# Performance work log

Hardware: AMD Instinct MI355X
Metric: run time of the kernel (lower is better)

Reference implementation:

```python
import jax, jax.numpy as jnp
import numpy as np

B, N, F, H = 8, 384, 64, 128
LN_EPS = 1e-5


def setup_inputs() -> dict:
    key = jax.random.key(0)
    ks = jax.random.split(key, 8)
    s = 0.1
    return {
        "inputs": jax.random.normal(ks[0], (B, N, F), jnp.float32),
        "positions": jax.random.normal(ks[1], (B, N, 3), jnp.float32),
        "vW1": jax.random.normal(ks[2], (2, H), jnp.float32) * s,
        "vb1": jnp.zeros((H,), jnp.float32),
        "vg": jnp.ones((H,), jnp.float32),
        "vbeta": jnp.zeros((H,), jnp.float32),
        "vW2": jax.random.normal(ks[3], (H, F), jnp.float32) * s,
        "vb2": jnp.zeros((F,), jnp.float32),
        "sW1": jax.random.normal(ks[4], (F, H), jnp.float32) * s,
        "sb1": jnp.zeros((H,), jnp.float32),
        "sW2": jax.random.normal(ks[5], (H, 1), jnp.float32) * s,
        "sb2": jnp.zeros((1,), jnp.float32),
    }


def reference(inputs, positions, vW1, vb1, vg, vbeta, vW2, vb2, sW1, sb1, sW2, sb2):
    # --- pairwise geometric invariants (rank=2, 'single'): [dot, |cross|] ---
    # left[b,i,j] = pos[b,j], right[b,i,j] = pos[b,i]
    dot = jnp.einsum("bjd,bid->bij", positions, positions)            # (B,N,N)
    cross = jnp.cross(positions[:, None, :, :], positions[:, :, None, :])
    cnorm = jnp.sqrt(jnp.sum(cross * cross, axis=-1))                  # (B,N,N)
    invariants = jnp.stack([dot, cnorm], axis=-1)                      # (B,N,N,2)

    # --- value_net: Linear -> LayerNorm -> ReLU -> Linear ---
    h = invariants @ vW1 + vb1                                         # (B,N,N,H)
    mu = jnp.mean(h, axis=-1, keepdims=True)
    var = jnp.mean((h - mu) ** 2, axis=-1, keepdims=True)
    h = (h - mu) * jax.lax.rsqrt(var + LN_EPS) * vg + vbeta
    invariant_values = jax.nn.relu(h) @ vW2 + vb2                      # (B,N,N,F)

    # --- merge ('mean') and join ('mean') ---
    merged = (inputs[:, None, :, :] + inputs[:, :, None, :]) * 0.5     # (B,N,N,F)
    joined = (invariant_values + merged) * 0.5                         # (B,N,N,F)

    # --- score_net: Linear -> ReLU -> Linear ---
    scores = jax.nn.relu(joined @ sW1 + sb1) @ sW2 + sb2               # (B,N,N,1)

    # --- flattened softmax over all N*N pairs, weighted sum over dim=-2 ---
    att = jax.nn.softmax(scores.reshape(scores.shape[0], -1), axis=-1)
    att = att.reshape(scores.shape)                                    # (B,N,N,1)
    x = jnp.sum(att * joined, axis=-2)                                 # (B,N,F)
    return x, att
```

## Files before the change

### kernel.cpp

```cpp
#include <hip/hip_runtime.h>
#include <hip/hip_bf16.h>
#include <math.h>

#define B_ 8
#define N_ 384
#define F_ 64
#define H_ 128
#define LN_EPS 1e-5f

typedef _Float16 f16;
typedef f16 f16x2 __attribute__((ext_vector_type(2)));
typedef f16 f16x4 __attribute__((ext_vector_type(4)));
typedef f16 f16x8 __attribute__((ext_vector_type(8)));
typedef float f32x4v __attribute__((ext_vector_type(4)));

static __device__ __forceinline__ f16x2 u2h(unsigned int u) {
    union { unsigned int u; f16x2 h; } c; c.u = u; return c.h;
}
static __device__ __forceinline__ unsigned int h2u(f16 a, f16 b) {
    union { f16x2 h; unsigned int u; } c; c.h = (f16x2){a, b}; return c.u;
}
static __device__ __forceinline__ unsigned int x2u(f16x2 h) {
    union { f16x2 h; unsigned int u; } c; c.h = h; return c.u;
}
static __device__ __forceinline__ f16x2 pk2(float a, float b) {
    auto r = __builtin_amdgcn_cvt_pkrtz(a, b);
    union { decltype(r) r; f16x2 h; } c; c.r = r; return c.h;
}

static __device__ __forceinline__ void perm_idx(int m, int& u, int& n0) {
    int h4 = (m >> 1) & 3, mf = m >> 3, p = m & 1;
    u = h4 * 16 + mf * 2 + p;
    n0 = mf * 16 + h4 * 4 + 2 * p;
}

__global__ __launch_bounds__(128) void k_prep(
    const float* __restrict__ inp, const float* __restrict__ sW1,
    const float* __restrict__ vb2, const float* __restrict__ sb1,
    const float* __restrict__ vW2, const float* __restrict__ vW1,
    const float* __restrict__ vb1, const float* __restrict__ vg,
    const float* __restrict__ vbeta, const float* __restrict__ sW2,
    unsigned int* __restrict__ t16, unsigned short* __restrict__ W2hT,
    unsigned int* __restrict__ coeffP, float* __restrict__ scal,
    unsigned int* __restrict__ sw16) {
    __shared__ float red[128];
    __shared__ float caS[128], cbS[128], ccS[128];
    const int bx = blockIdx.x;
    const int tid = threadIdx.x;

    if (bx < B_ * N_) {
        int row = bx, n = tid;
        float acc = 0.f;
#pragma unroll
        for (int f = 0; f < F_; ++f)
            acc = fmaf(0.25f * (inp[row * F_ + f] + vb2[f]), sW1[f * H_ + n], acc);
        red[n] = acc + 0.5f * sb1[n];
        __syncthreads();
        if (tid < 64) {
            int u, n0; perm_idx(tid, u, n0);
            t16[row * 64 + u] = h2u((f16)red[n0], (f16)red[n0 + 1]);
        }
        return;
    }
    if (bx < B_ * N_ + 128) {
        int idx = (bx - B_ * N_) * 128 + tid;
        int k = idx >> 7, n = idx & 127;
        float acc = 0.f;
#pragma unroll
        for (int f = 0; f < F_; ++f) acc = fmaf(vW2[k * F_ + f], sW1[f * H_ + n], acc);
        f16 hv = (f16)(0.5f * acc);
        W2hT[n * H_ + k] = *reinterpret_cast<unsigned short*>(&hv);
        return;
    }

    const int d = tid;
    float a = vW1[d], bb = vW1[H_ + d], c = vb1[d];
    float mA, mB, mC, Saa, Sbb, Scc, Sab, Sac, Sbc;
    float ca, cb, cc;
#define BMEAN(OUT, VAL)                                                  \
    red[d] = (VAL); __syncthreads();                                     \
    for (int st = 64; st > 0; st >>= 1) {                                \
        if (d < st) red[d] += red[d + st];                               \
        __syncthreads();                                                 \
    }                                                                    \
    OUT = red[0] * (1.f / 128.f); __syncthreads();

    BMEAN(mA, a); BMEAN(mB, bb); BMEAN(mC, c);
    ca = a - mA; cb = bb - mB; cc = c - mC;
    caS[d] = ca * vg[d]; cbS[d] = cb * vg[d]; ccS[d] = cc * vg[d];
    BMEAN(Saa, ca * ca); BMEAN(Sbb, cb * cb); BMEAN(Scc, cc * cc);
    BMEAN(Sab, ca * cb); BMEAN(Sac, ca * cc); BMEAN(Sbc, cb * cc);
#undef BMEAN
    __syncthreads();
    if (d < 64) {
        int d0 = 2 * d;
        coeffP[d]       = h2u((f16)caS[d0], (f16)caS[d0 + 1]);
        coeffP[64 + d]  = h2u((f16)cbS[d0], (f16)cbS[d0 + 1]);
        coeffP[128 + d] = h2u((f16)ccS[d0], (f16)ccS[d0 + 1]);
        coeffP[192 + d] = h2u((f16)vbeta[d0], (f16)vbeta[d0 + 1]);
        int u, n0; perm_idx(d, u, n0);
        sw16[u] = h2u((f16)sW2[n0], (f16)sW2[n0 + 1]);
    }
    if (d == 0) {
        scal[0] = Saa; scal[1] = Sbb; scal[2] = Scc;
        scal[3] = Sab; scal[4] = Sac; scal[5] = Sbc;
    }
}

#define VW2_OFF 32768
__global__ __launch_bounds__(256) void k_scores(
    const float* __restrict__ pos, const unsigned int* __restrict__ coeffP,
    const float* __restrict__ scal, const unsigned short* __restrict__ W2hT,
    const float* __restrict__ vW2, const unsigned int* __restrict__ t16,
    const unsigned int* __restrict__ sw16, const float* __restrict__ sb2,
    float* __restrict__ scores, float* __restrict__ rowsum,
    float* __restrict__ xpart) {
    __shared__ __align__(16) char smem[65536];

    const int tid = threadIdx.x;
    const int b = blockIdx.y;
    const int w = tid >> 6, lane = tid & 63;
    const int i = blockIdx.x * 4 + w;
    const int ln = lane & 15, h4 = lane >> 4;

#pragma unroll
    for (int s = 0; s < 8; ++s) {
        int idx = tid + s * 256;
        int n = idx >> 4, c = idx & 15;
        uint4 v = *(const uint4*)(W2hT + n * H_ + c * 8);
        *(uint4*)(smem + ((n * 256 + c * 16) ^ ((n & 7) << 4))) = v;
    }
#pragma unroll
    for (int s = 0; s < 8; ++s) {
        int idx = tid + s * 256;
        uint4 v = *(const uint4*)((const float*)vW2 + idx * 4);
        *(uint4*)(smem + VW2_OFF + idx * 16) = v;
    }
    __syncthreads();

    uint4 cagR[4], cbgR[4], ccgR[4], vbR[4];
#pragma unroll
    for (int kc = 0; kc < 4; ++kc) {
        cagR[kc] = *(const uint4*)(coeffP + kc * 16 + h4 * 4);
        cbgR[kc] = *(const uint4*)(coeffP + 64 + kc * 16 + h4 * 4);
        ccgR[kc] = *(const uint4*)(coeffP + 128 + kc * 16 + h4 * 4);
        vbR[kc]  = *(const uint4*)(coeffP + 192 + kc * 16 + h4 * 4);
    }
    f32x4v acc0[8];
    {
        const unsigned int* tiP = t16 + (size_t)(b * N_ + i) * 64 + h4 * 16;
#pragma unroll
        for (int s = 0; s < 4; ++s) {
            uint4 v = *(const uint4*)(tiP + s * 4);
            f16x2 a0 = u2h(v.x), a1 = u2h(v.y), a2 = u2h(v.z), a3 = u2h(v.w);
            acc0[s * 2][0] = (float)a0[0]; acc0[s * 2][1] = (float)a0[1];
            acc0[s * 2][2] = (float)a1[0]; acc0[s * 2][3] = (float)a1[1];
            acc0[s * 2 + 1][0] = (float)a2[0]; acc0[s * 2 + 1][1] = (float)a2[1];
            acc0[s * 2 + 1][2] = (float)a3[0]; acc0[s * 2 + 1][3] = (float)a3[1];
        }
    }
    uint2 swR[8];
#pragma unroll
    for (int mf = 0; mf < 8; ++mf)
        swR[mf] = *(const uint2*)(sw16 + h4 * 16 + mf * 2);

    const float Saa = scal[0], Sbb = scal[1], Scc = scal[2];
    const float Sab = scal[3], Sac = scal[4], Sbc = scal[5];
    const float sb2v = sb2[0];

    const float* pi = pos + (size_t)(b * N_ + i) * 3;
    const float ax = pi[0], ay = pi[1], az = pi[2];
    float* scoreRow = scores + (size_t)(b * N_ + i) * N_;

    float s_run = 0.f;
    unsigned int accPh[16];
#pragma unroll
    for (int k = 0; k < 16; ++k) accPh[k] = 0u;

    auto makeBF = [&](float bx_, float by_, float bz_, f16x8 (&bF)[4]) {
        float dotv = ax * bx_ + ay * by_ + az * bz_;
        float cx = ay * bz_ - az * by_;
        float cy = az * bx_ - ax * bz_;
        float cz = ax * by_ - ay * bx_;
        float cns = cx * cx + cy * cy + cz * cz;
        float cn = sqrtf(cns);
        float var = Saa * dotv * dotv + Sbb * cns + Scc +
                    2.f * (Sab * dotv * cn + Sac * dotv + Sbc * cn);
        float rstd = rsqrtf(var + LN_EPS);
        f16 d2 = (f16)(dotv * rstd), c2 = (f16)(cn * rstd), r2 = (f16)rstd;
        f16x2 D2 = {d2, d2}, C2 = {c2, c2}, R2 = {r2, r2};
        const f16x2 Z = {(f16)0.f, (f16)0.f};
#pragma unroll
        for (int kc = 0; kc < 4; ++kc) {
            f16x2 vp0 = __builtin_elementwise_max(D2 * u2h(cagR[kc].x) + (C2 * u2h(cbgR[kc].x) + (R2 * u2h(ccgR[kc].x) + u2h(vbR[kc].x))), Z);
            f16x2 vp1 = __builtin_elementwise_max(D2 * u2h(cagR[kc].y) + (C2 * u2h(cbgR[kc].y) + (R2 * u2h(ccgR[kc].y) + u2h(vbR[kc].y))), Z);
            f16x2 vp2 = __builtin_elementwise_max(D2 * u2h(cagR[kc].z) + (C2 * u2h(cbgR[kc].z) + (R2 * u2h(ccgR[kc].z) + u2h(vbR[kc].z))), Z);
            f16x2 vp3 = __builtin_elementwise_max(D2 * u2h(cagR[kc].w) + (C2 * u2h(cbgR[kc].w) + (R2 * u2h(ccgR[kc].w) + u2h(vbR[kc].w))), Z);
            f16x4 q01 = __builtin_shufflevector(vp0, vp1, 0, 1, 2, 3);
            f16x4 q23 = __builtin_shufflevector(vp2, vp3, 0, 1, 2, 3);
            bF[kc] = __builtin_shufflevector(q01, q23, 0, 1, 2, 3, 4, 5, 6, 7);
        }
    };

    float bx, by, bz;
    auto body = [&](int jt, f16x8 (&bFu)[4], f16x8 (&bFb)[4]) {
        const int j0 = jt * 16;

        const unsigned int* tjP = t16 + (size_t)(b * N_ + j0 + ln) * 64 + h4 * 16;
        uint4 tj0 = *(const uint4*)(tjP);
        uint4 tj1 = *(const uint4*)(tjP + 4);
        uint4 tj2 = *(const uint4*)(tjP + 8);
        uint4 tj3 = *(const uint4*)(tjP + 12);

        f32x4v acc[8];
        {
            const int kb = (h4 * 16) ^ ((ln & 7) << 4);
#pragma unroll
            for (int mf = 0; mf < 8; ++mf) {
                f16x8 aFr = *(const f16x8*)(smem + (mf * 16 + ln) * 256 + kb);
                acc[mf] = __builtin_amdgcn_mfma_f32_16x16x32_f16(aFr, bFu[0], acc0[mf], 0, 0, 0);
            }
        }
#pragma unroll
        for (int kc = 1; kc < 4; ++kc) {
            const int kb = (kc * 64 + h4 * 16) ^ ((ln & 7) << 4);
#pragma unroll
            for (int mf = 0; mf < 8; ++mf) {
                f16x8 aFr = *(const f16x8*)(smem + (mf * 16 + ln) * 256 + kb);
                acc[mf] = __builtin_amdgcn_mfma_f32_16x16x32_f16(aFr, bFu[kc], acc[mf], 0, 0, 0);
            }
        }

        {
            float gx = bx, gy = by, gz = bz;
            int jn2 = (jt + 2 < 24) ? (jt + 2) : 23;
            const float* pn = pos + (size_t)(b * N_ + jn2 * 16 + ln) * 3;
            bx = pn[0]; by = pn[1]; bz = pn[2];
            makeBF(gx, gy, gz, bFb);
        }

        unsigned int tju[16] = {tj0.x, tj0.y, tj0.z, tj0.w, tj1.x, tj1.y, tj1.z, tj1.w,
                                tj2.x, tj2.y, tj2.z, tj2.w, tj3.x, tj3.y, tj3.z, tj3.w};
        const f16x2 Z = {(f16)0.f, (f16)0.f};
        f16x2 psA = Z, psB = Z;
#pragma unroll
        for (int mf = 0; mf < 8; ++mf) {
            f16x2 p01 = pk2(acc[mf][0], acc[mf][1]);
            f16x2 p23 = pk2(acc[mf][2], acc[mf][3]);
            f16x2 r01 = __builtin_elementwise_max(p01 + u2h(tju[mf * 2]), Z);
            f16x2 r23 = __builtin_elementwise_max(p23 + u2h(tju[mf * 2 + 1]), Z);
            if (mf < 4) {
                psA = r01 * u2h(swR[mf].x) + (r23 * u2h(swR[mf].y) + psA);
            } else {
                psB = r01 * u2h(swR[mf].x) + (r23 * u2h(swR[mf].y) + psB);
            }
        }
        f16x2 ps = psA + psB;
        float part = (float)ps[0] + (float)ps[1];
        part += __shfl_xor(part, 16);
        part += __shfl_xor(part, 32);
        float sc = part + sb2v;
        if (h4 == 0) scoreRow[j0 + ln] = sc;

        float a = __expf(sc);
        s_run += a;
        {
            f16 ah = (f16)a;
            f16x2 A2 = {ah, ah};
#pragma unroll
            for (int kc = 0; kc < 4; ++kc) {
                union { f16x8 v; uint4 u; } bc; bc.v = bFu[kc];
                accPh[kc * 4 + 0] = x2u(u2h(bc.u.x) * A2 + u2h(accPh[kc * 4 + 0]));
                accPh[kc * 4 + 1] = x2u(u2h(bc.u.y) * A2 + u2h(accPh[kc * 4 + 1]));
                accPh[kc * 4 + 2] = x2u(u2h(bc.u.z) * A2 + u2h(accPh[kc * 4 + 2]));
                accPh[kc * 4 + 3] = x2u(u2h(bc.u.w) * A2 + u2h(accPh[kc * 4 + 3]));
            }
        }
    };

    f16x8 bFA[4], bFB[4];
    {
        const float* p0 = pos + (size_t)(b * N_ + ln) * 3;
        bx = p0[0]; by = p0[1]; bz = p0[2];
    }
    makeBF(bx, by, bz, bFA);
    {
        const float* p1 = pos + (size_t)(b * N_ + 16 + ln) * 3;
        bx = p1[0]; by = p1[1]; bz = p1[2];
    }

#pragma unroll 1
    for (int t = 0; t < 12; ++t) {
        body(2 * t, bFA, bFB);
        body(2 * t + 1, bFB, bFA);
    }

    float accH[4][8];
#pragma unroll
    for (int kc = 0; kc < 4; ++kc)
#pragma unroll
        for (int p = 0; p < 4; ++p) {
            f16x2 v = u2h(accPh[kc * 4 + p]);
            accH[kc][2 * p] = (float)v[0];
            accH[kc][2 * p + 1] = (float)v[1];
        }

#pragma unroll
    for (int d = 1; d < 16; d <<= 1) {
        s_run += __shfl_xor(s_run, d);
#pragma unroll
        for (int kc = 0; kc < 4; ++kc)
#pragma unroll
            for (int e = 0; e < 8; ++e) accH[kc][e] += __shfl_xor(accH[kc][e], d);
    }
    if (lane == 0) rowsum[b * N_ + i] = s_run;

    float xp0 = 0.f, xp1 = 0.f, xp2 = 0.f, xp3 = 0.f;
#pragma unroll
    for (int kc = 0; kc < 4; ++kc) {
#pragma unroll
        for (int e = 0; e < 8; ++e) {
            int dIdx = kc * 32 + h4 * 8 + e;
            float av = accH[kc][e];
            float4 wv = *(const float4*)(smem + VW2_OFF + dIdx * 256 + ln * 16);
            xp0 = fmaf(av, wv.x, xp0); xp1 = fmaf(av, wv.y, xp1);
            xp2 = fmaf(av, wv.z, xp2); xp3 = fmaf(av, wv.w, xp3);
        }
    }
    xp0 += __shfl_xor(xp0, 16); xp0 += __shfl_xor(xp0, 32);
    xp1 += __shfl_xor(xp1, 16); xp1 += __shfl_xor(xp1, 32);
    xp2 += __shfl_xor(xp2, 16); xp2 += __shfl_xor(xp2, 32);
    xp3 += __shfl_xor(xp3, 16); xp3 += __shfl_xor(xp3, 32);
    if (h4 == 0) {
        float4 o = {xp0, xp1, xp2, xp3};
        *(float4*)(xpart + (size_t)(b * N_ + i) * F_ + ln * 4) = o;
    }
}

__global__ void k_gred(const float* __restrict__ rowsum, float* __restrict__ invT) {
    int b = blockIdx.x, tid = threadIdx.x;
    __shared__ float sred[512];
    float s = (tid < N_) ? rowsum[b * N_ + tid] : 0.f;
    sred[tid] = s;
    __syncthreads();
    for (int st = 256; st > 0; st >>= 1) {
        if (tid < st) sred[tid] += sred[tid + st];
        __syncthreads();
    }
    if (tid == 0) invT[b] = 1.f / sred[0];
}

__global__ __launch_bounds__(256) void k_xlite(
    const float* __restrict__ inp, const float* __restrict__ vb2,
    float* __restrict__ scoresAtt, const float* __restrict__ rowsum,
    const float* __restrict__ invT, const float* __restrict__ xpart,
    float* __restrict__ xout) {
    int i = blockIdx.x, b = blockIdx.y;
    int tid = threadIdx.x;
    __shared__ float aLds[N_];
    __shared__ float accIp[256];

    const float invTb = invT[b];
    float* scoreRow = scoresAtt + (size_t)(b * N_ + i) * N_;

    {
        float sc = scoreRow[tid];
        float a = __expf(sc) * invTb;
        scoreRow[tid] = a; aLds[tid] = a;
        if (tid < N_ - 256) {
            float sc2 = scoreRow[tid + 256];
            float a2 = __expf(sc2) * invTb;
            scoreRow[tid + 256] = a2; aLds[tid + 256] = a2;
        }
    }
    __syncthreads();

    int f = tid & 63, q = tid >> 6;
    float aI = 0.f;
    const float* inB = inp + (size_t)b * N_ * F_;
    for (int j = q * 96; j < q * 96 + 96; ++j)
        aI = fmaf(aLds[j], inB[j * F_ + f], aI);
    accIp[tid] = aI;
    __syncthreads();

    if (tid < F_) {
        float accI = accIp[tid] + accIp[64 + tid] + accIp[128 + tid] + accIp[192 + tid];
        float s = rowsum[b * N_ + i] * invTb;
        float xp = xpart[(size_t)(b * N_ + i) * F_ + tid] * invTb;
        float r = 0.5f * (xp + s * vb2[tid]) +
                  0.25f * (s * inB[(size_t)i * F_ + tid] + accI);
        xout[(size_t)(b * N_ + i) * F_ + tid] = r;
    }
}


extern "C" void kernel_launch(void* const* d_in, const int* in_sizes, int n_in,
                              void* d_out, int out_size, void* d_ws, size_t ws_size,
                              hipStream_t stream) {
    const float* inp   = (const float*)d_in[0];
    const float* pos   = (const float*)d_in[1];
    const float* vW1   = (const float*)d_in[2];
    const float* vb1   = (const float*)d_in[3];
    const float* vg    = (const float*)d_in[4];
    const float* vbeta = (const float*)d_in[5];
    const float* vW2   = (const float*)d_in[6];
    const float* vb2   = (const float*)d_in[7];
    const float* sW1   = (const float*)d_in[8];
    const float* sb1   = (const float*)d_in[9];
    const float* sW2   = (const float*)d_in[10];
    const float* sb2   = (const float*)d_in[11];

    float* xout   = (float*)d_out;
    float* attout = xout + B_ * N_ * F_;

    unsigned short* W2hT   = (unsigned short*)d_ws;
    unsigned int*   coeffP = (unsigned int*)((char*)d_ws + 32768);
    float*          scal   = (float*)((char*)d_ws + 33792);
    unsigned int*   sw16   = (unsigned int*)((char*)d_ws + 34048);
    unsigned int*   t16    = (unsigned int*)((char*)d_ws + 34304);
    float* rowsum   = (float*)((char*)d_ws + 34304 + B_ * N_ * 64 * 4);
    float* invT     = rowsum + B_ * N_;
    float* xpart    = invT + B_;

    k_prep<<<B_ * N_ + 128 + 1, 128, 0, stream>>>(
        inp, sW1, vb2, sb1, vW2, vW1, vb1, vg, vbeta, sW2,
        t16, W2hT, coeffP, scal, sw16);
    k_scores<<<dim3(96, B_), 256, 0, stream>>>(
        pos, coeffP, scal, W2hT, vW2, t16, sw16, sb2, attout, rowsum, xpart);
    k_gred<<<B_, 512, 0, stream>>>(rowsum, invT);
    k_xlite<<<dim3(N_, B_), 256, 0, stream>>>(inp, vb2, attout, rowsum, invT,
                                              xpart, xout);
}
```

Measured before the change: 121.2 us.

## Fold global softmax-sum reduction into xlite kernel and prioritize MFMA block

Removes the separate k_gred launch. Each k_xlite block now recomputes the per-batch sum of 384 row sums itself through a small shared-memory tree and takes its reciprocal. In k_scores the MFMA loop gets precomputed swizzled LDS base pointers and is wrapped in s_setprio(1)/s_setprio(0) to raise wave priority during the matrix phase. This saves one kernel launch and a dependency, but every one of the 3072 xlite blocks repeats the 384-element reduction with three extra barriers.

```diff
diff --git a/kernel.cpp b/kernel.cpp
--- a/kernel.cpp
+++ b/kernel.cpp
@@ -172,6 +172,12 @@
     const float ax = pi[0], ay = pi[1], az = pi[2];
     float* scoreRow = scores + (size_t)(b * N_ + i) * N_;
 
+    const char* aBase = smem + ln * 256 + ((h4 * 16) ^ ((ln & 7) << 4));
+    const char* aBaseK[4];
+#pragma unroll
+    for (int kc = 0; kc < 4; ++kc)
+        aBaseK[kc] = smem + ln * 256 + ((kc * 64 + h4 * 16) ^ ((ln & 7) << 4));
+
     float s_run = 0.f;
     unsigned int accPh[16];
 #pragma unroll
@@ -212,24 +218,22 @@
         uint4 tj2 = *(const uint4*)(tjP + 8);
         uint4 tj3 = *(const uint4*)(tjP + 12);
 
+        __builtin_amdgcn_s_setprio(1);
         f32x4v acc[8];
-        {
-            const int kb = (h4 * 16) ^ ((ln & 7) << 4);
+#pragma unroll
+        for (int mf = 0; mf < 8; ++mf) {
+            f16x8 aFr = *(const f16x8*)(aBaseK[0] + mf * 4096);
+            acc[mf] = __builtin_amdgcn_mfma_f32_16x16x32_f16(aFr, bFu[0], acc0[mf], 0, 0, 0);
+        }
+#pragma unroll
+        for (int kc = 1; kc < 4; ++kc) {
 #pragma unroll
             for (int mf = 0; mf < 8; ++mf) {
-                f16x8 aFr = *(const f16x8*)(smem + (mf * 16 + ln) * 256 + kb);
-                acc[mf] = __builtin_amdgcn_mfma_f32_16x16x32_f16(aFr, bFu[0], acc0[mf], 0, 0, 0);
-            }
-        }
-#pragma unroll
-        for (int kc = 1; kc < 4; ++kc) {
-            const int kb = (kc * 64 + h4 * 16) ^ ((ln & 7) << 4);
-#pragma unroll
-            for (int mf = 0; mf < 8; ++mf) {
-                f16x8 aFr = *(const f16x8*)(smem + (mf * 16 + ln) * 256 + kb);
+                f16x8 aFr = *(const f16x8*)(aBaseK[kc] + mf * 4096);
                 acc[mf] = __builtin_amdgcn_mfma_f32_16x16x32_f16(aFr, bFu[kc], acc[mf], 0, 0, 0);
             }
         }
+        __builtin_amdgcn_s_setprio(0);
 
         {
             float gx = bx, gy = by, gz = bz;
@@ -337,30 +341,38 @@
     }
 }
 
-__global__ void k_gred(const float* __restrict__ rowsum, float* __restrict__ invT) {
-    int b = blockIdx.x, tid = threadIdx.x;
-    __shared__ float sred[512];
-    float s = (tid < N_) ? rowsum[b * N_ + tid] : 0.f;
-    sred[tid] = s;
-    __syncthreads();
-    for (int st = 256; st > 0; st >>= 1) {
-        if (tid < st) sred[tid] += sred[tid + st];
-        __syncthreads();
-    }
-    if (tid == 0) invT[b] = 1.f / sred[0];
-}
-
 __global__ __launch_bounds__(256) void k_xlite(
     const float* __restrict__ inp, const float* __restrict__ vb2,
     float* __restrict__ scoresAtt, const float* __restrict__ rowsum,
-    const float* __restrict__ invT, const float* __restrict__ xpart,
-    float* __restrict__ xout) {
+    const float* __restrict__ xpart, float* __restrict__ xout) {
     int i = blockIdx.x, b = blockIdx.y;
     int tid = threadIdx.x;
     __shared__ float aLds[N_];
     __shared__ float accIp[256];
-
-    const float invTb = invT[b];
+    __shared__ float tred[64];
+
+    {
+        int lane = tid & 63;
+        if (tid < 64) {
+            float s = 0.f;
+#pragma unroll
+            for (int k = 0; k < 6; ++k) s += rowsum[b * N_ + lane * 6 + k];
+            tred[lane] = s;
+        }
+        __syncthreads();
+        if (tid < 8) {
+            float s = tred[tid * 8] + tred[tid * 8 + 1] + tred[tid * 8 + 2] + tred[tid * 8 + 3]
+                    + tred[tid * 8 + 4] + tred[tid * 8 + 5] + tred[tid * 8 + 6] + tred[tid * 8 + 7];
+            tred[tid] = s;
+        }
+        __syncthreads();
+        if (tid == 0) {
+            float T = tred[0] + tred[1] + tred[2] + tred[3] + tred[4] + tred[5] + tred[6] + tred[7];
+            tred[0] = 1.f / T;
+        }
+        __syncthreads();
+    }
+    const float invTb = tred[0];
     float* scoreRow = scoresAtt + (size_t)(b * N_ + i) * N_;
 
     {
@@ -419,15 +431,12 @@
     unsigned int*   sw16   = (unsigned int*)((char*)d_ws + 34048);
     unsigned int*   t16    = (unsigned int*)((char*)d_ws + 34304);
     float* rowsum   = (float*)((char*)d_ws + 34304 + B_ * N_ * 64 * 4);
-    float* invT     = rowsum + B_ * N_;
-    float* xpart    = invT + B_;
+    float* xpart    = rowsum + B_ * N_;
 
     k_prep<<<B_ * N_ + 128 + 1, 128, 0, stream>>>(
         inp, sW1, vb2, sb1, vW2, vW1, vb1, vg, vbeta, sW2,
         t16, W2hT, coeffP, scal, sw16);
     k_scores<<<dim3(96, B_), 256, 0, stream>>>(
         pos, coeffP, scal, W2hT, vW2, t16, sw16, sb2, attout, rowsum, xpart);
-    k_gred<<<B_, 512, 0, stream>>>(rowsum, invT);
-    k_xlite<<<dim3(N_, B_), 256, 0, stream>>>(inp, vb2, attout, rowsum, invT,
-                                              xpart, xout);
-}
+    k_xlite<<<dim3(N_, B_), 256, 0, stream>>>(inp, vb2, attout, rowsum, xpart, xout);
+}
```

Result: faster. 109.3 us (-9.8%).
